# Kernel optimization log

Hardware: AMD Instinct MI355X
Metric: run time of the kernel (lower is better)

The kernel has to match this reference:

```python
import jax, jax.numpy as jnp
import numpy as np
from jax import lax

BS = 16; NG = 512; L = 2048; HOP = 512; ZD = 128; HD = 512
FS = L // 2 + 1
TAR = (NG - 1) * HOP + L  # 263680, matches int((NG+3)/4*L)
PPC = 5; PPK = 65
LOG10 = float(np.log(10.0))

def _hann_periodic(n):
    return (0.5 * (1.0 - np.cos(2.0 * np.pi * np.arange(n) / n))).astype(np.float32)

# filter window: fftshift(hann_window(L)) (torch periodic hann)
_FW = jnp.asarray(np.fft.fftshift(_hann_periodic(L)))
# OLA windows with edge correction (first/last grain half set to center value 1.0)
_w = _hann_periodic(L)
_ow = np.tile(_w[None, :], (NG, 1))
_ow[0, : L // 2] = _w[L // 2]
_ow[-1, L // 2 :] = _w[L // 2]
_OLA_W = jnp.asarray(_ow)  # [NG, L]
# overlap-add scatter indices and divisor (fold(unfold(ones)))
_IDX = jnp.asarray((np.arange(NG)[:, None] * HOP + np.arange(L)[None, :]).reshape(-1))
_DIV = jnp.zeros((TAR,), jnp.float32).at[_IDX].add(1.0)


def setup_inputs() -> dict:
    key = jax.random.key(0)
    ks = jax.random.split(key, 8)
    s = 0.02
    d = {}
    d["z"] = jax.random.normal(ks[0], (BS * NG, ZD), jnp.float32)
    d["w0"] = jax.random.normal(ks[1], (ZD, HD), jnp.float32) * s
    d["b0"] = jnp.zeros((HD,), jnp.float32)
    d["g0"] = jnp.ones((HD,), jnp.float32)
    d["be0"] = jnp.zeros((HD,), jnp.float32)
    d["w1"] = jax.random.normal(ks[2], (HD, HD), jnp.float32) * s
    d["b1"] = jnp.zeros((HD,), jnp.float32)
    d["g1"] = jnp.ones((HD,), jnp.float32)
    d["be1"] = jnp.zeros((HD,), jnp.float32)
    d["w2"] = jax.random.normal(ks[3], (HD, HD), jnp.float32) * s
    d["b2"] = jnp.zeros((HD,), jnp.float32)
    d["g2"] = jnp.ones((HD,), jnp.float32)
    d["be2"] = jnp.zeros((HD,), jnp.float32)
    d["w3"] = jax.random.normal(ks[4], (HD, FS), jnp.float32) * s
    d["b3"] = jnp.zeros((FS,), jnp.float32)
    d["pp_w"] = jax.random.normal(ks[5], (1, PPC, PPK), jnp.float32) * s
    d["pp_b"] = jnp.zeros((1,), jnp.float32)
    d["noise"] = jax.random.uniform(ks[6], (BS * NG, L), jnp.float32) * 2.0 - 1.0
    return d


def _lin_bn_lrelu(x, w, b, g, be):
    h = x @ w + b
    m = h.mean(0)
    v = jnp.mean((h - m) ** 2, 0)  # biased var (train-mode BatchNorm1d)
    h = (h - m) * lax.rsqrt(v + 1e-5) * g + be
    return jnp.where(h >= 0, h, 0.2 * h)  # LeakyReLU(0.2)


def reference(z, w0, b0, g0, be0, w1, b1, g1, be1, w2, b2, g2, be2, w3, b3, pp_w, pp_b, noise):
    # decoder MLP -> filter coefficients
    h = _lin_bn_lrelu(z, w0, b0, g0, be0)
    h = _lin_bn_lrelu(h, w1, b1, g1, be1)
    h = _lin_bn_lrelu(h, w2, b2, g2, be2)
    fc = h @ w3 + b3  # [BS*NG, FS]
    fc = 2.0 * jax.nn.sigmoid(fc) ** LOG10 + 1e-7  # mod_sigmoid
    # noise filtering in spectral domain
    ir = jnp.fft.irfft(fc.astype(jnp.complex64), n=L, axis=-1).astype(jnp.float32)
    ir = jnp.fft.fftshift(ir * _FW[None, :], axes=-1)
    audio = jnp.fft.irfft(jnp.fft.rfft(noise, axis=-1) * jnp.fft.rfft(ir, axis=-1), n=L, axis=-1).astype(jnp.float32)
    # per-grain windowing + overlap-add (nn.Fold equivalent scatter-add)
    audio = audio.reshape(BS, NG, L) * _OLA_W[None]
    audio_sum = jnp.zeros((BS, TAR), jnp.float32).at[:, _IDX].add(audio.reshape(BS, -1))
    audio_sum = audio_sum / _DIV  # normalize_ola
    # post-processing conv (PPC replicated channels -> 1) + softsign
    x = jnp.broadcast_to(audio_sum[:, None, :], (BS, PPC, TAR))
    y = lax.conv_general_dilated(x, pp_w, (1,), [(PPK // 2, PPK // 2)], dimension_numbers=("NCH", "OIH", "NCH"))
    y = y[:, 0, :] + pp_b[0]
    return y / (1.0 + jnp.abs(y))
```

## Files before the change

### kernel.cpp

```cpp
#include <hip/hip_runtime.h>
#include <hip/hip_bf16.h>
#include <math.h>

#define TARLEN 263680
#define POWEXP 2.302585092994046f
#define PC(i) ((i) + ((i) >> 3))

typedef __attribute__((ext_vector_type(8))) short bf16x8;
typedef __attribute__((ext_vector_type(8))) ushort u16x8;
typedef __attribute__((ext_vector_type(4))) float f32x4;

__device__ __forceinline__ void gload16(const void* g, void* l) {
    __builtin_amdgcn_global_load_lds((const __attribute__((address_space(1))) void*)g,
                                     (__attribute__((address_space(3))) void*)l, 16, 0, 0);
}

__device__ __forceinline__ float bf16f(ushort u) {
    union { uint u; float f; } v; v.u = (uint)u << 16; return v.f;
}
__device__ __forceinline__ ushort fbf16(float x) {
    __hip_bfloat16 h = __float2bfloat16(x);
    return *reinterpret_cast<ushort*>(&h);
}

__device__ __forceinline__ float vsin_rev(float rev) {
    float r; asm("v_sin_f32 %0, %1" : "=v"(r) : "v"(rev)); return r;
}
__device__ __forceinline__ float vcos_rev(float rev) {
    float r; asm("v_cos_f32 %0, %1" : "=v"(r) : "v"(rev)); return r;
}

__global__ __launch_bounds__(512) void gemm8(
    const ushort* __restrict__ A, const ushort* __restrict__ Bt,
    const float* __restrict__ bias, ushort* __restrict__ C,
    int K, float* __restrict__ ps, float* __restrict__ pq)
{
    __shared__ ushort As[3][4096];
    __shared__ ushort Bs[3][4096];
    __shared__ float sred[8][2][16];
    __shared__ float qred[8][2][16];
    const int tid = threadIdx.x;
    const int lane = tid & 63;
    const int wid = tid >> 6;
    const int nwg = gridDim.x * gridDim.y;
    const int bid = blockIdx.y * gridDim.x + blockIdx.x;
    const int q8 = nwg >> 3;
    const int swzb = (bid & 7) * q8 + (bid >> 3);
    const int bx = swzb % gridDim.x;
    const int by = swzb / gridDim.x;
    const int m0 = by * 128;
    const int n0 = bx * 128;
    const int NT = K >> 5;

    f32x4 acc[4][2];
#pragma unroll
    for (int m = 0; m < 4; ++m)
#pragma unroll
        for (int n = 0; n < 2; ++n)
            acc[m][n] = (f32x4){0.f, 0.f, 0.f, 0.f};

    const int srow = tid >> 2;
    const int scol = (((tid & 3) ^ ((tid >> 3) & 3)) << 3);

    auto stage = [&](int t, int buf) {
        const int k0 = t << 5;
        gload16(A + (size_t)(m0 + srow) * K + k0 + scol, &As[buf][tid * 8]);
        gload16(Bt + (size_t)(n0 + srow) * K + k0 + scol, &Bs[buf][tid * 8]);
    };

    const int lr = lane & 15;
    const int sw8 = (((lane >> 4) ^ ((lane >> 1) & 3)) << 3);
    const int wm0 = (wid >> 2) * 64;
    const int wn0 = (wid & 3) * 32;

    stage(0, 0);
    stage(1, 1);
    for (int t = 0; t < NT; ++t) {
        const int cur = t % 3;
        if (t + 2 < NT) {
            asm volatile("s_waitcnt vmcnt(2)" ::: "memory");
            __builtin_amdgcn_s_barrier();
            stage(t + 2, (t + 2) % 3);
        } else {
            asm volatile("s_waitcnt vmcnt(0)" ::: "memory");
            __builtin_amdgcn_s_barrier();
        }
        const ushort* as = As[cur];
        const ushort* bs = Bs[cur];
        bf16x8 af[4], bfv[2];
#pragma unroll
        for (int m = 0; m < 4; ++m)
            af[m] = *reinterpret_cast<const bf16x8*>(&as[(wm0 + m * 16 + lr) * 32 + sw8]);
#pragma unroll
        for (int n = 0; n < 2; ++n)
            bfv[n] = *reinterpret_cast<const bf16x8*>(&bs[(wn0 + n * 16 + lr) * 32 + sw8]);
#pragma unroll
        for (int m = 0; m < 4; ++m)
#pragma unroll
            for (int n = 0; n < 2; ++n)
                acc[m][n] = __builtin_amdgcn_mfma_f32_16x16x32_bf16(af[m], bfv[n], acc[m][n], 0, 0, 0);
    }
    __syncthreads();

    const int cr = (lane >> 4) << 2;
    const int cc = lane & 15;
    float sacc[2] = {0.f, 0.f}, qacc[2] = {0.f, 0.f};
#pragma unroll
    for (int m = 0; m < 4; ++m) {
#pragma unroll
        for (int n = 0; n < 2; ++n) {
            int gcol = n0 + wn0 + n * 16 + cc;
            float bv = bias[gcol];
            int grow = m0 + wm0 + m * 16 + cr;
#pragma unroll
            for (int j = 0; j < 4; ++j) {
                float v = acc[m][n][j] + bv;
                sacc[n] += v;
                qacc[n] += v * v;
                C[(size_t)(grow + j) * 512 + gcol] = fbf16(v);
            }
        }
    }
#pragma unroll
    for (int n = 0; n < 2; ++n) {
        float s = sacc[n], q = qacc[n];
        s += __shfl_xor(s, 16); q += __shfl_xor(q, 16);
        s += __shfl_xor(s, 32); q += __shfl_xor(q, 32);
        if (lane < 16) { sred[wid][n][lane] = s; qred[wid][n][lane] = q; }
    }
    __syncthreads();
    if (tid < 128) {
        int wn_ = tid >> 5, n_ = (tid >> 4) & 1, cc_ = tid & 15;
        float s = sred[wn_][n_][cc_] + sred[4 + wn_][n_][cc_];
        float q = qred[wn_][n_][cc_] + qred[4 + wn_][n_][cc_];
        int col = n0 + wn_ * 32 + n_ * 16 + cc_;
        ps[(size_t)by * 512 + col] = s;
        pq[(size_t)by * 512 + col] = q;
    }
}

template<int EPI>
__global__ __launch_bounds__(512) void gemm8n(
    const ushort* __restrict__ H, const ushort* __restrict__ Bt,
    const float* __restrict__ bias,
    const float* __restrict__ psIn, const float* __restrict__ pqIn,
    const float* __restrict__ gamma, const float* __restrict__ beta,
    ushort* __restrict__ C, int K, int Nvalid, int ldc,
    float* __restrict__ psOut, float* __restrict__ pqOut)
{
    __shared__ ushort As[3][4096];
    __shared__ ushort Bs[3][4096];
    __shared__ uint sab[512];
    __shared__ float sred[8][2][16];
    __shared__ float qred[8][2][16];
    const int tid = threadIdx.x;
    const int lane = tid & 63;
    const int wid = tid >> 6;
    const int nwg = gridDim.x * gridDim.y;
    const int bid = blockIdx.y * gridDim.x + blockIdx.x;
    const int q8 = nwg >> 3;
    const int swzb = (bid & 7) * q8 + (bid >> 3);
    const int bx = swzb % gridDim.x;
    const int by = swzb / gridDim.x;
    const int m0 = by * 128;
    const int n0 = bx * 128;
    const int NT = K >> 5;

    {
        int c = tid;
        float s = 0.f, q = 0.f;
#pragma unroll 8
        for (int rg = 0; rg < 64; ++rg) { s += psIn[rg * 512 + c]; q += pqIn[rg * 512 + c]; }
        float m = s * (1.f / 8192.f);
        float v = q * (1.f / 8192.f) - m * m;
        float a = rsqrtf(v + 1e-5f) * gamma[c];
        float b = beta[c] - m * a;
        sab[c] = (uint)fbf16(a) | ((uint)fbf16(b) << 16);
    }

    f32x4 acc[4][2];
#pragma unroll
    for (int m = 0; m < 4; ++m)
#pragma unroll
        for (int n = 0; n < 2; ++n)
            acc[m][n] = (f32x4){0.f, 0.f, 0.f, 0.f};

    const int srow = tid >> 2;
    const int scol = (((tid & 3) ^ ((tid >> 3) & 3)) << 3);
    const int lr = lane & 15;
    const int sw8 = (((lane >> 4) ^ ((lane >> 1) & 3)) << 3);
    const int wm0 = (wid >> 2) * 64;
    const int wn0 = (wid & 3) * 32;

    const size_t arow = (size_t)(m0 + srow) * K + scol;
    const size_t brow = (size_t)(n0 + srow) * K + scol;

    auto stageB = [&](int t, int buf) {
        gload16(Bt + brow + (t << 5), &Bs[buf][tid * 8]);
    };
    auto loadA = [&](int t, u16x8& dst) {
        dst = *reinterpret_cast<const u16x8*>(H + arow + (t << 5));
    };

    __syncthreads();

    u16x8 a0, a1;
    stageB(0, 0); loadA(0, a0);
    stageB(1, 1); loadA(1, a1);

    auto iter = [&](int t, u16x8& ar) {
        const int cur = t % 3;
        if (t + 2 < NT) asm volatile("s_waitcnt vmcnt(2)" ::: "memory");
        else            asm volatile("s_waitcnt vmcnt(0)" ::: "memory");
        {
            const uint* pk = &sab[(t << 5) + scol];
            u16x8 o;
#pragma unroll
            for (int j = 0; j < 8; ++j) {
                uint w = pk[j];
                float a = bf16f((ushort)(w & 0xffffu));
                float b = bf16f((ushort)(w >> 16));
                float y = fmaf(bf16f(ar[j]), a, b);
                o[j] = fbf16(y >= 0.f ? y : 0.2f * y);
            }
            *reinterpret_cast<u16x8*>(&As[cur][tid * 8]) = o;
        }
        asm volatile("s_waitcnt lgkmcnt(0)" ::: "memory");
        __builtin_amdgcn_s_barrier();
        if (t + 2 < NT) { stageB(t + 2, (t + 2) % 3); loadA(t + 2, ar); }
        const ushort* as = As[cur];
        const ushort* bs = Bs[cur];
        bf16x8 af[4], bfv[2];
#pragma unroll
        for (int m = 0; m < 4; ++m)
            af[m] = *reinterpret_cast<const bf16x8*>(&as[(wm0 + m * 16 + lr) * 32 + sw8]);
#pragma unroll
        for (int n = 0; n < 2; ++n)
            bfv[n] = *reinterpret_cast<const bf16x8*>(&bs[(wn0 + n * 16 + lr) * 32 + sw8]);
#pragma unroll
        for (int m = 0; m < 4; ++m)
#pragma unroll
            for (int n = 0; n < 2; ++n)
                acc[m][n] = __builtin_amdgcn_mfma_f32_16x16x32_bf16(af[m], bfv[n], acc[m][n], 0, 0, 0);
    };

    for (int t = 0; t < NT; t += 2) { iter(t, a0); iter(t + 1, a1); }
    __syncthreads();

    const int cr = (lane >> 4) << 2;
    const int cc = lane & 15;
    float sacc[2] = {0.f, 0.f}, qacc[2] = {0.f, 0.f};
#pragma unroll
    for (int m = 0; m < 4; ++m) {
#pragma unroll
        for (int n = 0; n < 2; ++n) {
            int gcol = n0 + wn0 + n * 16 + cc;
            if (EPI == 0 || gcol < Nvalid) {
                float bv = bias[gcol];
                int grow = m0 + wm0 + m * 16 + cr;
#pragma unroll
                for (int j = 0; j < 4; ++j) {
                    float v = acc[m][n][j] + bv;
                    if (EPI == 1) {
                        float sg = 1.f / (1.f + __expf(-v));
                        v = 2.f * __expf(POWEXP * __logf(sg)) + 1e-7f;
                    } else {
                        sacc[n] += v;
                        qacc[n] += v * v;
                    }
                    C[(size_t)(grow + j) * ldc + gcol] = fbf16(v);
                }
            }
        }
    }
    if (EPI == 0) {
#pragma unroll
        for (int n = 0; n < 2; ++n) {
            float s = sacc[n], q = qacc[n];
            s += __shfl_xor(s, 16); q += __shfl_xor(q, 16);
            s += __shfl_xor(s, 32); q += __shfl_xor(q, 32);
            if (lane < 16) { sred[wid][n][lane] = s; qred[wid][n][lane] = q; }
        }
        __syncthreads();
        if (tid < 128) {
            int wn_ = tid >> 5, n_ = (tid >> 4) & 1, cc_ = tid & 15;
            float s = sred[wn_][n_][cc_] + sred[4 + wn_][n_][cc_];
            float q = qred[wn_][n_][cc_] + qred[4 + wn_][n_][cc_];
            int col = n0 + wn_ * 32 + n_ * 16 + cc_;
            psOut[(size_t)by * 512 + col] = s;
            pqOut[(size_t)by * 512 + col] = q;
        }
    }
}

__global__ __launch_bounds__(256) void prep_inputs(
    const float* __restrict__ w0, const float* __restrict__ w1,
    const float* __restrict__ w2, const float* __restrict__ w3,
    const float* __restrict__ z,
    ushort* __restrict__ B0, ushort* __restrict__ B1,
    ushort* __restrict__ B2, ushort* __restrict__ B3,
    ushort* __restrict__ A)
{
    if (blockIdx.z == 4) {
        int bid = blockIdx.y * gridDim.x + blockIdx.x;
        if (bid >= 512) return;
        int idx = (bid * 256 + threadIdx.x) << 3;
        float4 a = *reinterpret_cast<const float4*>(&z[idx]);
        float4 b = *reinterpret_cast<const float4*>(&z[idx + 4]);
        float x[8] = {a.x, a.y, a.z, a.w, b.x, b.y, b.z, b.w};
        u16x8 o;
#pragma unroll
        for (int j = 0; j < 8; ++j) o[j] = fbf16(x[j]);
        *reinterpret_cast<u16x8*>(&A[idx]) = o;
        return;
    }
    const float* w; ushort* Bt; int K, N, GX, GY;
    switch (blockIdx.z) {
        case 0: w = w0; Bt = B0; K = 128; N = 512;  GX = 4;  GY = 16; break;
        case 1: w = w1; Bt = B1; K = 512; N = 512;  GX = 16; GY = 16; break;
        case 2: w = w2; Bt = B2; K = 512; N = 512;  GX = 16; GY = 16; break;
        default:w = w3; Bt = B3; K = 512; N = 1025; GX = 16; GY = 36; break;
    }
    if ((int)blockIdx.x >= GX || (int)blockIdx.y >= GY) return;
    __shared__ float tile[32][33];
    int k0 = blockIdx.x * 32, n0 = blockIdx.y * 32;
    int tx = threadIdx.x & 31, ty = threadIdx.x >> 5;
#pragma unroll
    for (int r = 0; r < 4; ++r) {
        int k = k0 + ty + r * 8;
        int n = n0 + tx;
        tile[ty + r * 8][tx] = (n < N) ? w[(size_t)k * N + n] : 0.f;
    }
    __syncthreads();
#pragma unroll
    for (int r = 0; r < 4; ++r) {
        int n = n0 + ty + r * 8;
        int k = k0 + tx;
        Bt[(size_t)n * K + k] = fbf16(tile[tx][ty + r * 8]);
    }
}

__device__ __forceinline__ float2 cmul(float2 a, float c, float s) {
    return make_float2(a.x * c - a.y * s, a.x * s + a.y * c);
}

template<bool INV, int L>
__device__ __forceinline__ void stk_stage(
    const float2* __restrict__ s, float2* __restrict__ d, int t)
{
    int k = t & (L - 1);
    float2 x0 = s[PC(t)];
    float2 x1 = s[PC(t + 256)];
    float2 x2 = s[PC(t + 512)];
    float2 x3 = s[PC(t + 768)];
    if (L > 1) {
        float rev = (float)k * (1.0f / (float)(4 * L));
        float s1 = vsin_rev(rev), c1 = vcos_rev(rev);
        if (!INV) s1 = -s1;
        float c2 = c1 * c1 - s1 * s1, s2 = 2.f * c1 * s1;
        float c3 = c2 * c1 - s2 * s1, s3 = s2 * c1 + c2 * s1;
        x1 = cmul(x1, c1, s1);
        x2 = cmul(x2, c2, s2);
        x3 = cmul(x3, c3, s3);
    }
    float2 a = make_float2(x0.x + x2.x, x0.y + x2.y);
    float2 b = make_float2(x0.x - x2.x, x0.y - x2.y);
    float2 c = make_float2(x1.x + x3.x, x1.y + x3.y);
    float2 e = make_float2(x1.x - x3.x, x1.y - x3.y);
    int db = ((t - k) << 2) + k;
    d[PC(db)]         = make_float2(a.x + c.x, a.y + c.y);
    d[PC(db + 2 * L)] = make_float2(a.x - c.x, a.y - c.y);
    if (!INV) {
        d[PC(db + L)]     = make_float2(b.x + e.y, b.y - e.x);
        d[PC(db + 3 * L)] = make_float2(b.x - e.y, b.y + e.x);
    } else {
        d[PC(db + L)]     = make_float2(b.x - e.y, b.y + e.x);
        d[PC(db + 3 * L)] = make_float2(b.x + e.y, b.y - e.x);
    }
}

__global__ __launch_bounds__(256) void fft_filter_kernel(
    const float* __restrict__ noise, const ushort* __restrict__ fcsb,
    ushort* __restrict__ awb)
{
    __shared__ float2 X[1152], Y[1152];
    __shared__ float F[1025];
    const int tid = threadIdx.x;
    const int r = blockIdx.x;

    const float2* nrow = reinterpret_cast<const float2*>(noise + ((size_t)r << 11));
    for (int i = tid; i < 1025; i += 256) F[i] = bf16f(fcsb[(size_t)r * 1040 + i]);
    {
        float2 x0 = nrow[tid], x1 = nrow[tid + 256], x2 = nrow[tid + 512], x3 = nrow[tid + 768];
        float2 a = make_float2(x0.x + x2.x, x0.y + x2.y);
        float2 b = make_float2(x0.x - x2.x, x0.y - x2.y);
        float2 c = make_float2(x1.x + x3.x, x1.y + x3.y);
        float2 e = make_float2(x1.x - x3.x, x1.y - x3.y);
        int db = tid << 2;
        Y[PC(db)]     = make_float2(a.x + c.x, a.y + c.y);
        Y[PC(db + 1)] = make_float2(b.x + e.y, b.y - e.x);
        Y[PC(db + 2)] = make_float2(a.x - c.x, a.y - c.y);
        Y[PC(db + 3)] = make_float2(b.x - e.y, b.y + e.x);
    }
    __syncthreads();
    stk_stage<false, 4>(Y, X, tid);   __syncthreads();
    stk_stage<false, 16>(X, Y, tid);  __syncthreads();
    stk_stage<false, 64>(Y, X, tid);  __syncthreads();
    stk_stage<false, 256>(X, Y, tid); __syncthreads();

    const float INV1024 = 1.0f / 1024.0f;
    auto proc = [&](int k, float c, float s) {
        int k2 = (1024 - k) & 1023;
        float2 za = Y[PC(k)], zb = Y[PC(k2)];
        float Fer = 0.5f * (za.x + zb.x), Fei = 0.5f * (za.y - zb.y);
        float For = 0.5f * (za.y + zb.y), Foi = 0.5f * (zb.x - za.x);
        float wFr = c * For - s * Foi;
        float wFi = c * Foi + s * For;
        float Xkr = Fer + wFr, Xki = Fei + wFi;
        float Xbr = Fer - wFr, Xbi = wFi - Fei;
        float Hk, Hb;
        {
            float cl = (k == 0) ? F[1] : F[k - 1];
            float crr = (k == 1024) ? F[1023] : F[k + 1];
            float h = 0.5f * F[k] + 0.25f * (cl + crr);
            Hk = ((k & 1) ? -h : h) * INV1024;
        }
        {
            int kb = 1024 - k;
            float cl = (kb == 0) ? F[1] : F[kb - 1];
            float crr = (kb == 1024) ? F[1023] : F[kb + 1];
            float h = 0.5f * F[kb] + 0.25f * (cl + crr);
            Hb = ((kb & 1) ? -h : h) * INV1024;
        }
        float Ykr = Hk * Xkr, Yki = Hk * Xki;
        float Ybr = Hb * Xbr, Ybi = Hb * Xbi;
        if (k == 0) {
            X[PC(0)] = make_float2(0.5f * (Ykr + Ybr), 0.5f * (Ykr - Ybr));
        } else {
            float Ger = 0.5f * (Ykr + Ybr), Gei = 0.5f * (Yki - Ybi);
            float Sgr = 0.5f * (Ykr - Ybr), Sgi = 0.5f * (Yki + Ybi);
            float wpr = c, wpi = -s;
            float Gor = wpr * Sgr - wpi * Sgi;
            float Goi = wpr * Sgi + wpi * Sgr;
            X[PC(k)]  = make_float2(Ger - Goi, Gei + Gor);
            X[PC(k2)] = make_float2(Ger + Goi, Gor - Gei);
        }
    };
    {
        float rev0 = (float)tid * (1.0f / 2048.0f);
        float c0 = vcos_rev(rev0), s0 = -vsin_rev(rev0);
        proc(tid, c0, s0);
        float rev1 = (float)(tid + 256) * (1.0f / 2048.0f);
        float c1 = vcos_rev(rev1), s1 = -vsin_rev(rev1);
        proc(tid + 256, c1, s1);
        if (tid == 0) proc(512, 0.f, -1.f);
    }
    __syncthreads();

    stk_stage<true, 1>(X, Y, tid);  __syncthreads();
    stk_stage<true, 4>(Y, X, tid);  __syncthreads();
    stk_stage<true, 16>(X, Y, tid); __syncthreads();
    stk_stage<true, 64>(Y, X, tid); __syncthreads();

    {
        const int g = r & 511;
        ushort2* awrow = reinterpret_cast<ushort2*>(awb + ((size_t)r << 11));
        int t = tid;
        float2 x0 = X[PC(t)], x1 = X[PC(t + 256)], x2 = X[PC(t + 512)], x3 = X[PC(t + 768)];
        float rev = (float)t * (1.0f / 1024.0f);
        float s1 = vsin_rev(rev), c1 = vcos_rev(rev);
        float c2 = c1 * c1 - s1 * s1, s2 = 2.f * c1 * s1;
        float c3 = c2 * c1 - s2 * s1, s3 = s2 * c1 + c2 * s1;
        x1 = cmul(x1, c1, s1);
        x2 = cmul(x2, c2, s2);
        x3 = cmul(x3, c3, s3);
        float2 a = make_float2(x0.x + x2.x, x0.y + x2.y);
        float2 b = make_float2(x0.x - x2.x, x0.y - x2.y);
        float2 c = make_float2(x1.x + x3.x, x1.y + x3.y);
        float2 e = make_float2(x1.x - x3.x, x1.y - x3.y);
        float2 o[4];
        o[0] = make_float2(a.x + c.x, a.y + c.y);
        o[1] = make_float2(b.x - e.y, b.y + e.x);
        o[2] = make_float2(a.x - c.x, a.y - c.y);
        o[3] = make_float2(b.x + e.y, b.y - e.x);
        float cq[4] = {c1, -s1, -c1, s1};
        float sq[4] = {s1, c1, -s1, -c1};
        const float COSD = 0.99999529380958f;
        const float SIND = 0.00306795676296f;
#pragma unroll
        for (int q = 0; q < 4; ++q) {
            int n = t + 256 * q;
            float w0, w1;
            bool edge = (g == 0 && q < 2) || (g == 511 && q >= 2);
            if (edge) { w0 = 1.f; w1 = 1.f; }
            else {
                w0 = 0.5f - 0.5f * cq[q];
                w1 = 0.5f - 0.5f * (cq[q] * COSD - sq[q] * SIND);
            }
            ushort2 ov; ov.x = fbf16(o[q].x * w0); ov.y = fbf16(o[q].y * w1);
            awrow[n] = ov;
        }
    }
}

__global__ __launch_bounds__(256) void ola_ppconv_kernel(
    const ushort* __restrict__ awb, const float* __restrict__ ppw,
    const float* __restrict__ ppb, float* __restrict__ out)
{
    __shared__ float tile[320];
    __shared__ float Ksh[65];
    int t0 = blockIdx.x * 256;
    int b = blockIdx.y;
    const ushort* awbase = awb + ((size_t)(b * 512) << 11);
    for (int i = threadIdx.x; i < 320; i += 256) {
        int tt = t0 - 32 + i;
        float v = 0.f;
        if (tt >= 1536 && tt < 262144) {
            int glo = (tt - 1536) >> 9;
            const ushort* p = awbase + ((size_t)glo << 11) + (tt - (glo << 9));
            float s = bf16f(p[0]) + bf16f(p[1536]) + bf16f(p[3072]) + bf16f(p[4608]);
            v = s * 0.25f;
        } else if (tt >= 0 && tt < TARLEN) {
            int ghi = min(511, tt >> 9);
            int glo = max(0, (tt - 1536) >> 9);
            float s = 0.f;
            for (int g = glo; g <= ghi; ++g) {
                int n = tt - (g << 9);
                s += bf16f(awbase[((size_t)g << 11) + n]);
            }
            v = s / (float)(ghi - glo + 1);
        }
        tile[i] = v;
    }
    if (threadIdx.x < 65) {
        float k = 0.f;
#pragma unroll
        for (int c = 0; c < 5; ++c) k += ppw[c * 65 + threadIdx.x];
        Ksh[threadIdx.x] = k;
    }
    __syncthreads();
    float y = ppb[0];
#pragma unroll
    for (int j = 0; j < 65; ++j) y = fmaf(Ksh[j], tile[threadIdx.x + j], y);
    int t = t0 + threadIdx.x;
    out[(size_t)b * TARLEN + t] = y / (1.f + fabsf(y));
}

extern "C" void kernel_launch(void* const* d_in, const int* in_sizes, int n_in,
                              void* d_out, int out_size, void* d_ws, size_t ws_size,
                              hipStream_t stream) {
    const float* z    = (const float*)d_in[0];
    const float* w0   = (const float*)d_in[1];
    const float* b0   = (const float*)d_in[2];
    const float* g0   = (const float*)d_in[3];
    const float* be0  = (const float*)d_in[4];
    const float* w1   = (const float*)d_in[5];
    const float* b1   = (const float*)d_in[6];
    const float* g1   = (const float*)d_in[7];
    const float* be1  = (const float*)d_in[8];
    const float* w2   = (const float*)d_in[9];
    const float* b2   = (const float*)d_in[10];
    const float* g2   = (const float*)d_in[11];
    const float* be2  = (const float*)d_in[12];
    const float* w3   = (const float*)d_in[13];
    const float* b3   = (const float*)d_in[14];
    const float* ppw  = (const float*)d_in[15];
    const float* ppb  = (const float*)d_in[16];
    const float* noise= (const float*)d_in[17];
    float* out = (float*)d_out;
    float* ws = (float*)d_ws;

    ushort* h0b = (ushort*)ws;
    ushort* h1b = (ushort*)(ws + 2097152);
    float* ps0  = ws + 4194304;
    float* pq0  = ps0 + 32768;
    float* ps1  = pq0 + 32768;
    float* pq1  = ps1 + 32768;
    float* base = pq1 + 32768;
    ushort* Bt0 = (ushort*)base;
    ushort* Bt1 = (ushort*)(base + 32768);
    ushort* Bt2 = (ushort*)(base + 163840);
    ushort* Bt3 = (ushort*)(base + 294912);
    ushort* fcsb= (ushort*)(base + 589824);
    ushort* awb = (ushort*)(base + 4849664);
    ushort* A   = (ushort*)(base + 13238272);
    ushort* h2b = h0b;

    dim3 blk(256);
    dim3 gblk(512);
    prep_inputs<<<dim3(16, 36, 5), blk, 0, stream>>>(
        w0, w1, w2, w3, z, Bt0, Bt1, Bt2, Bt3, A);
    gemm8<<<dim3(4, 64), gblk, 0, stream>>>(A, Bt0, b0, h0b, 128, ps0, pq0);
    gemm8n<0><<<dim3(4, 64), gblk, 0, stream>>>(
        h0b, Bt1, b1, ps0, pq0, g0, be0, h1b, 512, 512, 512, ps1, pq1);
    gemm8n<0><<<dim3(4, 64), gblk, 0, stream>>>(
        h1b, Bt2, b2, ps1, pq1, g1, be1, h2b, 512, 512, 512, ps0, pq0);
    gemm8n<1><<<dim3(9, 64), gblk, 0, stream>>>(
        h2b, Bt3, b3, ps0, pq0, g2, be2, fcsb, 512, 1025, 1040, nullptr, nullptr);
    fft_filter_kernel<<<dim3(8192), blk, 0, stream>>>(noise, fcsb, awb);
    ola_ppconv_kernel<<<dim3(1030, 16), blk, 0, stream>>>(awb, ppw, ppb, out);
    (void)in_sizes; (void)n_in; (void)out_size; (void)ws_size;
}
```

Measured before the change: 159.1 us.

## Switch normalized GEMMs to 64x128 tiles with 256-thread blocks

Replaces the 512-thread 128x128-tile GEMM used for layers 1-3 with a 256-thread 64x128-tile variant, doubling the grid in M so more workgroups fill the CUs. Each wave now covers all 64 rows, which removes the cross-wave LDS reduction and the extra barriers for the BN partial sums. Partial-sum buffers grow to 128 row groups, and the consumer loops over ngIn groups. The cost is more B-tile reloads per output, since B is fetched twice as often, and more partial-sum reduction work at the start of the next kernel.

```diff
diff --git a/kernel.cpp b/kernel.cpp
--- a/kernel.cpp
+++ b/kernel.cpp
@@ -140,19 +140,17 @@
 }
 
 template<int EPI>
-__global__ __launch_bounds__(512) void gemm8n(
+__global__ __launch_bounds__(256) void gemm4n(
     const ushort* __restrict__ H, const ushort* __restrict__ Bt,
     const float* __restrict__ bias,
-    const float* __restrict__ psIn, const float* __restrict__ pqIn,
+    const float* __restrict__ psIn, const float* __restrict__ pqIn, int ngIn,
     const float* __restrict__ gamma, const float* __restrict__ beta,
     ushort* __restrict__ C, int K, int Nvalid, int ldc,
     float* __restrict__ psOut, float* __restrict__ pqOut)
 {
-    __shared__ ushort As[3][4096];
+    __shared__ ushort As[3][2048];
     __shared__ ushort Bs[3][4096];
     __shared__ uint sab[512];
-    __shared__ float sred[8][2][16];
-    __shared__ float qred[8][2][16];
     const int tid = threadIdx.x;
     const int lane = tid & 63;
     const int wid = tid >> 6;
@@ -162,15 +160,14 @@
     const int swzb = (bid & 7) * q8 + (bid >> 3);
     const int bx = swzb % gridDim.x;
     const int by = swzb / gridDim.x;
-    const int m0 = by * 128;
+    const int m0 = by * 64;
     const int n0 = bx * 128;
     const int NT = K >> 5;
 
-    {
-        int c = tid;
+    for (int c = tid; c < 512; c += 256) {
         float s = 0.f, q = 0.f;
-#pragma unroll 8
-        for (int rg = 0; rg < 64; ++rg) { s += psIn[rg * 512 + c]; q += pqIn[rg * 512 + c]; }
+#pragma unroll 4
+        for (int rg = 0; rg < ngIn; ++rg) { s += psIn[rg * 512 + c]; q += pqIn[rg * 512 + c]; }
         float m = s * (1.f / 8192.f);
         float v = q * (1.f / 8192.f) - m * m;
         float a = rsqrtf(v + 1e-5f) * gamma[c];
@@ -189,14 +186,15 @@
     const int scol = (((tid & 3) ^ ((tid >> 3) & 3)) << 3);
     const int lr = lane & 15;
     const int sw8 = (((lane >> 4) ^ ((lane >> 1) & 3)) << 3);
-    const int wm0 = (wid >> 2) * 64;
-    const int wn0 = (wid & 3) * 32;
-
-    const size_t arow = (size_t)(m0 + srow) * K + scol;
-    const size_t brow = (size_t)(n0 + srow) * K + scol;
+    const int wn0 = wid * 32;
+
+    const size_t arow  = (size_t)(m0 + srow) * K + scol;
+    const size_t brow0 = (size_t)(n0 + srow) * K + scol;
+    const size_t brow1 = (size_t)(n0 + 64 + srow) * K + scol;
 
     auto stageB = [&](int t, int buf) {
-        gload16(Bt + brow + (t << 5), &Bs[buf][tid * 8]);
+        gload16(Bt + brow0 + (t << 5), &Bs[buf][tid * 8]);
+        gload16(Bt + brow1 + (t << 5), &Bs[buf][2048 + tid * 8]);
     };
     auto loadA = [&](int t, u16x8& dst) {
         dst = *reinterpret_cast<const u16x8*>(H + arow + (t << 5));
@@ -210,7 +208,7 @@
 
     auto iter = [&](int t, u16x8& ar) {
         const int cur = t % 3;
-        if (t + 2 < NT) asm volatile("s_waitcnt vmcnt(2)" ::: "memory");
+        if (t + 2 < NT) asm volatile("s_waitcnt vmcnt(3)" ::: "memory");
         else            asm volatile("s_waitcnt vmcnt(0)" ::: "memory");
         {
             const uint* pk = &sab[(t << 5) + scol];
@@ -233,7 +231,7 @@
         bf16x8 af[4], bfv[2];
 #pragma unroll
         for (int m = 0; m < 4; ++m)
-            af[m] = *reinterpret_cast<const bf16x8*>(&as[(wm0 + m * 16 + lr) * 32 + sw8]);
+            af[m] = *reinterpret_cast<const bf16x8*>(&as[(m * 16 + lr) * 32 + sw8]);
 #pragma unroll
         for (int n = 0; n < 2; ++n)
             bfv[n] = *reinterpret_cast<const bf16x8*>(&bs[(wn0 + n * 16 + lr) * 32 + sw8]);
@@ -245,7 +243,6 @@
     };
 
     for (int t = 0; t < NT; t += 2) { iter(t, a0); iter(t + 1, a1); }
-    __syncthreads();
 
     const int cr = (lane >> 4) << 2;
     const int cc = lane & 15;
@@ -257,7 +254,7 @@
             int gcol = n0 + wn0 + n * 16 + cc;
             if (EPI == 0 || gcol < Nvalid) {
                 float bv = bias[gcol];
-                int grow = m0 + wm0 + m * 16 + cr;
+                int grow = m0 + m * 16 + cr;
 #pragma unroll
                 for (int j = 0; j < 4; ++j) {
                     float v = acc[m][n][j] + bv;
@@ -279,16 +276,11 @@
             float s = sacc[n], q = qacc[n];
             s += __shfl_xor(s, 16); q += __shfl_xor(q, 16);
             s += __shfl_xor(s, 32); q += __shfl_xor(q, 32);
-            if (lane < 16) { sred[wid][n][lane] = s; qred[wid][n][lane] = q; }
-        }
-        __syncthreads();
-        if (tid < 128) {
-            int wn_ = tid >> 5, n_ = (tid >> 4) & 1, cc_ = tid & 15;
-            float s = sred[wn_][n_][cc_] + sred[4 + wn_][n_][cc_];
-            float q = qred[wn_][n_][cc_] + qred[4 + wn_][n_][cc_];
-            int col = n0 + wn_ * 32 + n_ * 16 + cc_;
-            psOut[(size_t)by * 512 + col] = s;
-            pqOut[(size_t)by * 512 + col] = q;
+            if (lane < 16) {
+                int col = n0 + wn0 + n * 16 + lane;
+                psOut[(size_t)by * 512 + col] = s;
+                pqOut[(size_t)by * 512 + col] = q;
+            }
         }
     }
 }
@@ -573,10 +565,10 @@
     ushort* h0b = (ushort*)ws;
     ushort* h1b = (ushort*)(ws + 2097152);
     float* ps0  = ws + 4194304;
-    float* pq0  = ps0 + 32768;
-    float* ps1  = pq0 + 32768;
-    float* pq1  = ps1 + 32768;
-    float* base = pq1 + 32768;
+    float* pq0  = ps0 + 65536;
+    float* ps1  = pq0 + 65536;
+    float* pq1  = ps1 + 65536;
+    float* base = pq1 + 65536;
     ushort* Bt0 = (ushort*)base;
     ushort* Bt1 = (ushort*)(base + 32768);
     ushort* Bt2 = (ushort*)(base + 163840);
@@ -591,12 +583,12 @@
     prep_inputs<<<dim3(16, 36, 5), blk, 0, stream>>>(
         w0, w1, w2, w3, z, Bt0, Bt1, Bt2, Bt3, A);
     gemm8<<<dim3(4, 64), gblk, 0, stream>>>(A, Bt0, b0, h0b, 128, ps0, pq0);
-    gemm8n<0><<<dim3(4, 64), gblk, 0, stream>>>(
-        h0b, Bt1, b1, ps0, pq0, g0, be0, h1b, 512, 512, 512, ps1, pq1);
-    gemm8n<0><<<dim3(4, 64), gblk, 0, stream>>>(
-        h1b, Bt2, b2, ps1, pq1, g1, be1, h2b, 512, 512, 512, ps0, pq0);
-    gemm8n<1><<<dim3(9, 64), gblk, 0, stream>>>(
-        h2b, Bt3, b3, ps0, pq0, g2, be2, fcsb, 512, 1025, 1040, nullptr, nullptr);
+    gemm4n<0><<<dim3(4, 128), blk, 0, stream>>>(
+        h0b, Bt1, b1, ps0, pq0, 64, g0, be0, h1b, 512, 512, 512, ps1, pq1);
+    gemm4n<0><<<dim3(4, 128), blk, 0, stream>>>(
+        h1b, Bt2, b2, ps1, pq1, 128, g1, be1, h2b, 512, 512, 512, ps0, pq0);
+    gemm4n<1><<<dim3(9, 128), blk, 0, stream>>>(
+        h2b, Bt3, b3, ps0, pq0, 128, g2, be2, fcsb, 512, 1025, 1040, nullptr, nullptr);
     fft_filter_kernel<<<dim3(8192), blk, 0, stream>>>(noise, fcsb, awb);
     ola_ppconv_kernel<<<dim3(1030, 16), blk, 0, stream>>>(awb, ppw, ppb, out);
     (void)in_sizes; (void)n_in; (void)out_size; (void)ws_size;
```

Result: slower. 211.5 us (+32.9%).
